# Kernel tuning notes

Hardware: AMD Instinct MI355X
Metric: run time of the kernel (lower is better)

The kernel has to match this reference:

```python
import jax, jax.numpy as jnp
import numpy as np

HEADS = 8
DK = 64            # key_size == size_per_head
NEIGHBORS = 3
KSIZE = 1 + 2 * NEIGHBORS  # 7 (rate=1)


def setup_inputs() -> dict:
    key = jax.random.key(0)
    k1, k2, k3, k4 = jax.random.split(key, 4)
    B, HW, S, D = 2, 64, 256, 512
    inputs = jax.random.normal(k1, (B, HW, S, D), dtype=jnp.float32)
    pos_bias = jax.random.normal(k2, (HEADS, S, KSIZE), dtype=jnp.float32)
    W_qkv = jax.random.normal(k3, (D, 3 * HEADS * DK), dtype=jnp.float32) * 0.02
    W_out = jax.random.normal(k4, (HEADS * DK, D), dtype=jnp.float32) * 0.02
    return {"inputs": inputs, "pos_bias": pos_bias, "W_qkv": W_qkv, "W_out": W_out}


def reference(inputs, pos_bias, W_qkv, W_out):
    B, HW, S, D = inputs.shape
    # qkv projection (no bias), split into q, k, v
    qkv = inputs @ W_qkv                                   # [B,HW,S,3*H*DK]
    q, k, v = jnp.split(qkv, 3, axis=-1)
    q = (q / jnp.sqrt(jnp.float32(DK))).reshape(B, HW, S, HEADS, DK)
    k = k.reshape(B, HW, S, HEADS, DK)
    v = v.reshape(B, HW, S, HEADS, DK)

    # zero-pad keys/values along seq (faithful to F.pad with value=0)
    pad = NEIGHBORS
    kp = jnp.pad(k, ((0, 0), (0, 0), (pad, pad), (0, 0), (0, 0)))
    vp = jnp.pad(v, ((0, 0), (0, 0), (pad, pad), (0, 0), (0, 0)))

    # sliding-window gather: window w for query i covers padded positions i..i+KSIZE-1
    idx = jnp.arange(S)[:, None] + jnp.arange(KSIZE)[None, :]  # [S,KSIZE]
    kw = kp[:, :, idx]                                         # [B,HW,S,KSIZE,H,DK]
    vw = vp[:, :, idx]                                         # [B,HW,S,KSIZE,H,DK]

    # scores over the window
    attn = jnp.einsum('bnshd,bnswhd->bnswh', q, kw)            # [B,HW,S,KSIZE,H]
    # additive positional bias: [H,S,KSIZE] -> [S,KSIZE,H] broadcast
    attn = attn + jnp.transpose(pos_bias, (1, 2, 0))[None, None]
    attn = jax.nn.softmax(attn, axis=-2)                       # softmax over window dim

    out = jnp.einsum('bnswh,bnswhd->bnshd', attn, vw)          # [B,HW,S,H,DK]
    out = out.reshape(B, HW, S, HEADS * DK)
    return out @ W_out
```

## Files before the change

### kernel.cpp

```cpp
#include <hip/hip_runtime.h>
#include <hip/hip_bf16.h>
#include <cstdint>


typedef __bf16 bf16x8 __attribute__((ext_vector_type(8)));
typedef float f32x4 __attribute__((ext_vector_type(4)));

__device__ __forceinline__ uint16_t f2bf(float f) {
    uint32_t u = __builtin_bit_cast(uint32_t, f);
    return (uint16_t)((u + 0x7fffu + ((u >> 16) & 1u)) >> 16);
}
__device__ __forceinline__ float bflo(uint32_t u) { return __builtin_bit_cast(float, u << 16); }
__device__ __forceinline__ float bfhi(uint32_t u) { return __builtin_bit_cast(float, u & 0xffff0000u); }

__device__ __forceinline__ void unpack8(uint4 v, float* f) {
    f[0] = bflo(v.x); f[1] = bfhi(v.x);
    f[2] = bflo(v.y); f[3] = bfhi(v.y);
    f[4] = bflo(v.z); f[5] = bfhi(v.z);
    f[6] = bflo(v.w); f[7] = bfhi(v.w);
}
__device__ __forceinline__ uint32_t pack2(float a, float b) {
    return (uint32_t)f2bf(a) | ((uint32_t)f2bf(b) << 16);
}

#define GLOAD_LDS16(gp, lp)                                                        \
    __builtin_amdgcn_global_load_lds((const __attribute__((address_space(1))) void*)(gp), \
                                     (__attribute__((address_space(3))) void*)(lp), 16, 0, 0)

__device__ __forceinline__ bf16x8 ds_read16(const uint16_t* p) {
    bf16x8 r;
    asm volatile("ds_read_b128 %0, %1"
                 : "=v"(r)
                 : "v"((const __attribute__((address_space(3))) void*)p));
    return r;
}

__global__ void cvt_f32_bf16(const float* __restrict__ in, uint16_t* __restrict__ out, int n8) {
    int i = blockIdx.x * 256 + threadIdx.x;
    if (i >= n8) return;
    const float4* p = (const float4*)in + (size_t)i * 2;
    float4 a = p[0], b = p[1];
    uint4 o;
    o.x = pack2(a.x, a.y);
    o.y = pack2(a.z, a.w);
    o.z = pack2(b.x, b.y);
    o.w = pack2(b.z, b.w);
    *((uint4*)out + i) = o;
}

__global__ void transpose_cvt(const float* __restrict__ in, uint16_t* __restrict__ out,
                              int R, int C) {
    int idx = blockIdx.x * 256 + threadIdx.x;
    if (idx >= R * C) return;
    int r = idx / C;
    int c = idx - r * C;
    out[(size_t)c * R + r] = f2bf(in[idx]);
}

template <bool F32OUT>
__global__ __launch_bounds__(512, 2)
void gemm256(const uint16_t* __restrict__ A, const uint16_t* __restrict__ BT,
             void* __restrict__ Cout, int M, int N, int K) {
    __shared__ __align__(16) uint16_t lds[65536];

    const int tid  = threadIdx.x;
    const int lane = tid & 63;
    const int wv   = tid >> 6;
    const int r    = lane & 15;
    const int quad = lane >> 4;
    const int wr   = wv >> 2;
    const int wc   = wv & 3;
    const long bm0 = (long)blockIdx.x * 256;
    const long bn0 = (long)blockIdx.y * 256;
    const int NT   = K >> 6;

    const int c0 = tid, c1 = tid + 512;
    const int row0 = c0 >> 3, row1 = c1 >> 3;
    const int sw0 = ((c0 & 7) ^ (row0 & 7)) * 8;
    const int sw1 = ((c1 & 7) ^ (row1 & 7)) * 8;
    const uint16_t* pA0 = A  + (bm0 + row0) * (long)K + sw0;
    const uint16_t* pA1 = A  + (bm0 + row1) * (long)K + sw1;
    const uint16_t* pB0 = BT + (bn0 + row0) * (long)K + sw0;
    const uint16_t* pB1 = BT + (bn0 + row1) * (long)K + sw1;
    const long hstep = 128 * (long)K;

#define STAGE_A(b_, h_, t_) do {                                                        \
        GLOAD_LDS16(pA0 + (h_) * hstep + (t_) * 64,                                     \
                    &lds[(b_) * 16384 + (h_) * 8192 + c0 * 8]);                         \
        GLOAD_LDS16(pA1 + (h_) * hstep + (t_) * 64,                                     \
                    &lds[(b_) * 16384 + (h_) * 8192 + c1 * 8]);                         \
    } while (0)
#define STAGE_B(b_, h_, t_) do {                                                        \
        GLOAD_LDS16(pB0 + (h_) * hstep + (t_) * 64,                                     \
                    &lds[32768 + (b_) * 16384 + (h_) * 8192 + c0 * 8]);                 \
        GLOAD_LDS16(pB1 + (h_) * hstep + (t_) * 64,                                     \
                    &lds[32768 + (b_) * 16384 + (h_) * 8192 + c1 * 8]);                 \
    } while (0)

    const int swk0 = ((0 + quad) ^ (r & 7)) * 8;
    const int swk1 = ((4 + quad) ^ (r & 7)) * 8;
    const int arow = (wr * 128 + r) * 64;
    const int brow = (wc * 64 + r) * 64;

#define DS_A(mf_, kk_) ds_read16(&lds[aoff + arow + (mf_) * 1024 + ((kk_) ? swk1 : swk0)])
#define DS_B(nf_, kk_) ds_read16(&lds[boff + brow + (nf_) * 1024 + ((kk_) ? swk1 : swk0)])

#define WAITK4 do { asm volatile("s_waitcnt lgkmcnt(4)" ::: "memory");                  \
                    __builtin_amdgcn_sched_barrier(0); } while (0)
#define WAITK0 do { asm volatile("s_waitcnt lgkmcnt(0)" ::: "memory");                  \
                    __builtin_amdgcn_sched_barrier(0); } while (0)

#define MFMA_CL(mbase_, ar_)                                                            \
    __builtin_amdgcn_s_setprio(1);                                                      \
    _Pragma("unroll")                                                                   \
    for (int kk = 0; kk < 2; ++kk)                                                      \
        _Pragma("unroll")                                                               \
        for (int mi = 0; mi < 2; ++mi)                                                  \
            _Pragma("unroll")                                                           \
            for (int nf = 0; nf < 4; ++nf)                                              \
                acc[(mbase_) + mi][nf] = __builtin_amdgcn_mfma_f32_16x16x32_bf16(       \
                    ar_[mi][kk], bfr[nf][kk], acc[(mbase_) + mi][nf], 0, 0, 0);         \
    __builtin_amdgcn_s_setprio(0);

    f32x4 acc[8][4];
#pragma unroll
    for (int mf = 0; mf < 8; ++mf)
#pragma unroll
        for (int nf = 0; nf < 4; ++nf) acc[mf][nf] = (f32x4){0.f, 0.f, 0.f, 0.f};

    STAGE_A(0, 0, 0); STAGE_A(0, 1, 0);
    STAGE_B(0, 0, 0); STAGE_B(0, 1, 0);
    asm volatile("s_waitcnt vmcnt(0)" ::: "memory");
    __builtin_amdgcn_s_barrier();

    for (int t = 0; t < NT; ++t) {
        const int b    = t & 1;
        const int aoff = b * 16384;
        const int boff = 32768 + b * 16384;
        const bool pf  = (t + 1 < NT);

        bf16x8 bfr[4][2];
        bf16x8 a0[2][2], a1[2][2];

#pragma unroll
        for (int nf = 0; nf < 4; ++nf) { bfr[nf][0] = DS_B(nf, 0); bfr[nf][1] = DS_B(nf, 1); }
        a0[0][0] = DS_A(0, 0); a0[0][1] = DS_A(0, 1);
        a0[1][0] = DS_A(1, 0); a0[1][1] = DS_A(1, 1);
        if (pf) { STAGE_A(b ^ 1, 0, t + 1); STAGE_B(b ^ 1, 0, t + 1); }

        a1[0][0] = DS_A(2, 0); a1[0][1] = DS_A(2, 1);
        a1[1][0] = DS_A(3, 0); a1[1][1] = DS_A(3, 1);
        if (pf) { STAGE_A(b ^ 1, 1, t + 1); STAGE_B(b ^ 1, 1, t + 1); }

        WAITK4;
        MFMA_CL(0, a0)

        a0[0][0] = DS_A(4, 0); a0[0][1] = DS_A(4, 1);
        a0[1][0] = DS_A(5, 0); a0[1][1] = DS_A(5, 1);
        WAITK4;
        MFMA_CL(2, a1)

        a1[0][0] = DS_A(6, 0); a1[0][1] = DS_A(6, 1);
        a1[1][0] = DS_A(7, 0); a1[1][1] = DS_A(7, 1);
        WAITK4;
        MFMA_CL(4, a0)

        WAITK0;
        MFMA_CL(6, a1)

        if (pf) {
            asm volatile("s_waitcnt vmcnt(0)" ::: "memory");
            __builtin_amdgcn_s_barrier();
        }
    }

#pragma unroll
    for (int mf = 0; mf < 8; ++mf) {
#pragma unroll
        for (int i = 0; i < 4; ++i) {
            long m = bm0 + wr * 128 + mf * 16 + quad * 4 + i;
            if (F32OUT) {
                float* crow = (float*)Cout + m * (long)N + bn0 + wc * 64 + r;
#pragma unroll
                for (int nf = 0; nf < 4; ++nf) crow[nf * 16] = acc[mf][nf][i];
            } else {
                uint16_t* crow = (uint16_t*)Cout + m * (long)N + bn0 + wc * 64 + r;
#pragma unroll
                for (int nf = 0; nf < 4; ++nf) crow[nf * 16] = f2bf(acc[mf][nf][i]);
            }
        }
    }
#undef STAGE_A
#undef STAGE_B
#undef DS_A
#undef DS_B
#undef WAITK4
#undef WAITK0
#undef MFMA_CL
}

__global__ __launch_bounds__(256, 2)
void local_attn(const uint16_t* __restrict__ qkv, const float* __restrict__ pb,
                uint16_t* __restrict__ attn) {
    __shared__ __align__(16) uint4 smem[4192];

    const int h  = blockIdx.x & 7;
    const int bn = blockIdx.x >> 3;
    const int s  = threadIdx.x;
    const int tid = threadIdx.x;
    const size_t base = (size_t)bn * 256 * 1536;

    const uint16_t* qrow = qkv + base + (size_t)s * 1536 + h * 64;
    uint4 qc[8];
#pragma unroll
    for (int c = 0; c < 8; ++c) qc[c] = *(const uint4*)(qrow + c * 8);

    if (tid < 96) {
        int a    = tid / 48;
        int rem  = tid - a * 48;
        int hr6  = rem >> 3;
        int c8   = rem & 7;
        int hrow = (hr6 < 3) ? hr6 : (256 + hr6);
        smem[a * 2096 + hrow * 8 + c8] = (uint4){0u, 0u, 0u, 0u};
    }

#pragma unroll
    for (int it = 0; it < 16; ++it) {
        int i   = tid + it * 256;
        int a   = i >> 11;
        int idx = i & 2047;
        int sp  = idx >> 3;
        int cs  = (i & 7) ^ ((sp + 3) & 7);
        const uint16_t* src = qkv + base + (size_t)sp * 1536 + 512 + a * 512 + h * 64 + cs * 8;
        GLOAD_LDS16(src, (uint16_t*)&smem[a * 2096 + (sp + 3) * 8 + (i & 7)]);
    }

    __syncthreads();

    float sc[7];
#pragma unroll
    for (int w = 0; w < 7; ++w) sc[w] = 0.f;

#pragma unroll
    for (int c = 0; c < 8; ++c) {
        float qf[8];
        unpack8(qc[c], qf);
        uint4 kc[7];
#pragma unroll
        for (int w = 0; w < 7; ++w) {
            int hrow = s + w;
            kc[w] = smem[hrow * 8 + (c ^ (hrow & 7))];
        }
#pragma unroll
        for (int w = 0; w < 7; ++w) {
            float kf[8];
            unpack8(kc[w], kf);
#pragma unroll
            for (int j = 0; j < 8; ++j) sc[w] += qf[j] * kf[j];
        }
    }

    const float* pbr = pb + ((size_t)h * 256 + s) * 7;
    float mx = -1e30f;
#pragma unroll
    for (int w = 0; w < 7; ++w) {
        sc[w] = sc[w] * 0.125f + pbr[w];
        mx = fmaxf(mx, sc[w]);
    }
    float p[7], sum = 0.f;
#pragma unroll
    for (int w = 0; w < 7; ++w) {
        p[w] = __expf(sc[w] - mx);
        sum += p[w];
    }
    const float inv = 1.f / sum;
#pragma unroll
    for (int w = 0; w < 7; ++w) p[w] *= inv;

    uint4 ov[8];
#pragma unroll
    for (int c = 0; c < 8; ++c) {
        uint4 vc[7];
#pragma unroll
        for (int w = 0; w < 7; ++w) {
            int hrow = s + w;
            vc[w] = smem[2096 + hrow * 8 + (c ^ (hrow & 7))];
        }
        float o[8] = {0.f, 0.f, 0.f, 0.f, 0.f, 0.f, 0.f, 0.f};
#pragma unroll
        for (int w = 0; w < 7; ++w) {
            float vf[8];
            unpack8(vc[w], vf);
#pragma unroll
            for (int j = 0; j < 8; ++j) o[j] += p[w] * vf[j];
        }
        ov[c].x = pack2(o[0], o[1]);
        ov[c].y = pack2(o[2], o[3]);
        ov[c].z = pack2(o[4], o[5]);
        ov[c].w = pack2(o[6], o[7]);
    }

    uint16_t* orow = attn + ((size_t)(bn * 256 + s)) * 512 + h * 64;
#pragma unroll
    for (int c = 0; c < 8; ++c) *(uint4*)(orow + c * 8) = ov[c];
}

extern "C" void kernel_launch(void* const* d_in, const int* in_sizes, int n_in,
                              void* d_out, int out_size, void* d_ws, size_t ws_size,
                              hipStream_t stream) {
    const float* X    = (const float*)d_in[0];
    const float* pb   = (const float*)d_in[1];
    const float* Wqkv = (const float*)d_in[2];
    const float* Wout = (const float*)d_in[3];
    float* out = (float*)d_out;

    char* ws = (char*)d_ws;
    uint16_t* WqkvT = (uint16_t*)(ws);
    uint16_t* WoutT = (uint16_t*)(ws + 1572864);
    uint16_t* qkvb  = (uint16_t*)(ws + 2097152);
    uint16_t* Xb    = (uint16_t*)(ws + 102760448);
    uint16_t* attnb = Xb;

    cvt_f32_bf16<<<(32768 * 512 / 8 + 255) / 256, 256, 0, stream>>>(X, Xb, 32768 * 512 / 8);
    transpose_cvt<<<(512 * 1536 + 255) / 256, 256, 0, stream>>>(Wqkv, WqkvT, 512, 1536);
    transpose_cvt<<<(512 * 512 + 255) / 256, 256, 0, stream>>>(Wout, WoutT, 512, 512);

    gemm256<false><<<dim3(128, 6), 512, 0, stream>>>(Xb, WqkvT, qkvb, 32768, 1536, 512);
    local_attn<<<1024, 256, 0, stream>>>(qkvb, pb, attnb);
    gemm256<true><<<dim3(128, 2), 512, 0, stream>>>(attnb, WoutT, out, 32768, 512, 512);
}
```

Baseline: 257.0 us.

## Shrink GEMM tiles to 256x128 with K=32 steps and split attention waits

The GEMM changes from 256x256 tiles with K-step 64 to 256x128 tiles with K-step 32. This cuts LDS use from 128KB to 48KB and raises the occupancy target to 4 blocks per CU. It also uses a new swizzle so each LDS row packs two tile rows, and it doubles the grid. In the local attention kernel, Q is loaded with explicit global loads and the barriers are split with vmcnt waits, so V staging can overlap the score computation. The smaller tiles give less reuse per block and more barriers per K.

Result: slower. 264.4 us (+2.9%).

```diff
diff --git a/kernel.cpp b/kernel.cpp
--- a/kernel.cpp
+++ b/kernel.cpp
@@ -32,6 +32,14 @@
     asm volatile("ds_read_b128 %0, %1"
                  : "=v"(r)
                  : "v"((const __attribute__((address_space(3))) void*)p));
+    return r;
+}
+
+__device__ __forceinline__ uint4 gload16(const uint16_t* p) {
+    uint4 r;
+    asm volatile("global_load_dwordx4 %0, %1, off"
+                 : "=v"(r)
+                 : "v"((const __attribute__((address_space(1))) void*)p));
     return r;
 }
 
@@ -58,115 +66,95 @@
 }
 
 template <bool F32OUT>
-__global__ __launch_bounds__(512, 2)
-void gemm256(const uint16_t* __restrict__ A, const uint16_t* __restrict__ BT,
+__global__ __launch_bounds__(512, 4)
+void gemm_mn(const uint16_t* __restrict__ A, const uint16_t* __restrict__ BT,
              void* __restrict__ Cout, int M, int N, int K) {
-    __shared__ __align__(16) uint16_t lds[65536];
+    __shared__ __align__(16) uint16_t lds[24576];
 
     const int tid  = threadIdx.x;
     const int lane = tid & 63;
     const int wv   = tid >> 6;
     const int r    = lane & 15;
     const int quad = lane >> 4;
-    const int wr   = wv >> 2;
-    const int wc   = wv & 3;
+    const int wr   = wv >> 1;
+    const int wc   = wv & 1;
     const long bm0 = (long)blockIdx.x * 256;
-    const long bn0 = (long)blockIdx.y * 256;
-    const int NT   = K >> 6;
-
-    const int c0 = tid, c1 = tid + 512;
-    const int row0 = c0 >> 3, row1 = c1 >> 3;
-    const int sw0 = ((c0 & 7) ^ (row0 & 7)) * 8;
-    const int sw1 = ((c1 & 7) ^ (row1 & 7)) * 8;
-    const uint16_t* pA0 = A  + (bm0 + row0) * (long)K + sw0;
-    const uint16_t* pA1 = A  + (bm0 + row1) * (long)K + sw1;
-    const uint16_t* pB0 = BT + (bn0 + row0) * (long)K + sw0;
-    const uint16_t* pB1 = BT + (bn0 + row1) * (long)K + sw1;
-    const long hstep = 128 * (long)K;
-
-#define STAGE_A(b_, h_, t_) do {                                                        \
-        GLOAD_LDS16(pA0 + (h_) * hstep + (t_) * 64,                                     \
-                    &lds[(b_) * 16384 + (h_) * 8192 + c0 * 8]);                         \
-        GLOAD_LDS16(pA1 + (h_) * hstep + (t_) * 64,                                     \
-                    &lds[(b_) * 16384 + (h_) * 8192 + c1 * 8]);                         \
+    const long bn0 = (long)blockIdx.y * 128;
+    const int NT   = K >> 5;
+
+#define SRC_ROWCOL(d_, row_, col_) do {                                                 \
+        int ln_ = (d_) >> 3, pre_ = ((d_) & 7) ^ (ln_ & 7);                             \
+        row_ = 2 * ln_ + (pre_ >> 2);                                                   \
+        col_ = (pre_ & 3) * 8;                                                          \
     } while (0)
-#define STAGE_B(b_, h_, t_) do {                                                        \
-        GLOAD_LDS16(pB0 + (h_) * hstep + (t_) * 64,                                     \
-                    &lds[32768 + (b_) * 16384 + (h_) * 8192 + c0 * 8]);                 \
-        GLOAD_LDS16(pB1 + (h_) * hstep + (t_) * 64,                                     \
-                    &lds[32768 + (b_) * 16384 + (h_) * 8192 + c1 * 8]);                 \
+    int rA0, cA0, rA1, cA1, rB0, cB0;
+    SRC_ROWCOL(tid,       rA0, cA0);
+    SRC_ROWCOL(tid + 512, rA1, cA1);
+    SRC_ROWCOL(tid,       rB0, cB0);
+    const uint16_t* pA0 = A  + (bm0 + rA0) * (long)K + cA0;
+    const uint16_t* pA1 = A  + (bm0 + rA1) * (long)K + cA1;
+    const uint16_t* pB0 = BT + (bn0 + rB0) * (long)K + cB0;
+#undef SRC_ROWCOL
+
+#define STAGE(b_, t_) do {                                                              \
+        GLOAD_LDS16(pA0 + (t_) * 32, &lds[(b_) * 8192 + tid * 8]);                      \
+        GLOAD_LDS16(pA1 + (t_) * 32, &lds[(b_) * 8192 + (tid + 512) * 8]);              \
+        GLOAD_LDS16(pB0 + (t_) * 32, &lds[16384 + (b_) * 4096 + tid * 8]);              \
     } while (0)
 
-    const int swk0 = ((0 + quad) ^ (r & 7)) * 8;
-    const int swk1 = ((4 + quad) ^ (r & 7)) * 8;
-    const int arow = (wr * 128 + r) * 64;
-    const int brow = (wc * 64 + r) * 64;
-
-#define DS_A(mf_, kk_) ds_read16(&lds[aoff + arow + (mf_) * 1024 + ((kk_) ? swk1 : swk0)])
-#define DS_B(nf_, kk_) ds_read16(&lds[boff + brow + (nf_) * 1024 + ((kk_) ? swk1 : swk0)])
-
-#define WAITK4 do { asm volatile("s_waitcnt lgkmcnt(4)" ::: "memory");                  \
+    const int p_ln  = (((r & 1) << 2) | quad) ^ ((r >> 1) & 7);
+    const int aLane = wr * 2048 + (r >> 1) * 64 + p_ln * 8;
+    const int bLane = 16384 + wc * 2048 + (r >> 1) * 64 + p_ln * 8;
+
+#define DS_A(mf_) ds_read16(&lds[aoff + aLane + (mf_) * 512])
+#define DS_B(nf_) ds_read16(&lds[boff + bLane + (nf_) * 512])
+
+#define WAITK2 do { asm volatile("s_waitcnt lgkmcnt(2)" ::: "memory");                  \
                     __builtin_amdgcn_sched_barrier(0); } while (0)
 #define WAITK0 do { asm volatile("s_waitcnt lgkmcnt(0)" ::: "memory");                  \
                     __builtin_amdgcn_sched_barrier(0); } while (0)
 
-#define MFMA_CL(mbase_, ar_)                                                            \
+#define MFMA_CL(m0_, f0_, f1_)                                                          \
     __builtin_amdgcn_s_setprio(1);                                                      \
     _Pragma("unroll")                                                                   \
-    for (int kk = 0; kk < 2; ++kk)                                                      \
-        _Pragma("unroll")                                                               \
-        for (int mi = 0; mi < 2; ++mi)                                                  \
-            _Pragma("unroll")                                                           \
-            for (int nf = 0; nf < 4; ++nf)                                              \
-                acc[(mbase_) + mi][nf] = __builtin_amdgcn_mfma_f32_16x16x32_bf16(       \
-                    ar_[mi][kk], bfr[nf][kk], acc[(mbase_) + mi][nf], 0, 0, 0);         \
+    for (int nf = 0; nf < 4; ++nf)                                                      \
+        acc[(m0_)][nf] = __builtin_amdgcn_mfma_f32_16x16x32_bf16(f0_, bfr[nf],          \
+                                                                 acc[(m0_)][nf], 0, 0, 0); \
+    _Pragma("unroll")                                                                   \
+    for (int nf = 0; nf < 4; ++nf)                                                      \
+        acc[(m0_) + 1][nf] = __builtin_amdgcn_mfma_f32_16x16x32_bf16(f1_, bfr[nf],      \
+                                                                 acc[(m0_) + 1][nf], 0, 0, 0); \
     __builtin_amdgcn_s_setprio(0);
 
-    f32x4 acc[8][4];
-#pragma unroll
-    for (int mf = 0; mf < 8; ++mf)
+    f32x4 acc[4][4];
+#pragma unroll
+    for (int mf = 0; mf < 4; ++mf)
 #pragma unroll
         for (int nf = 0; nf < 4; ++nf) acc[mf][nf] = (f32x4){0.f, 0.f, 0.f, 0.f};
 
-    STAGE_A(0, 0, 0); STAGE_A(0, 1, 0);
-    STAGE_B(0, 0, 0); STAGE_B(0, 1, 0);
+    STAGE(0, 0);
     asm volatile("s_waitcnt vmcnt(0)" ::: "memory");
     __builtin_amdgcn_s_barrier();
 
     for (int t = 0; t < NT; ++t) {
         const int b    = t & 1;
-        const int aoff = b * 16384;
-        const int boff = 32768 + b * 16384;
+        const int aoff = b * 8192;
+        const int boff = b * 4096;
         const bool pf  = (t + 1 < NT);
 
-        bf16x8 bfr[4][2];
-        bf16x8 a0[2][2], a1[2][2];
-
-#pragma unroll
-        for (int nf = 0; nf < 4; ++nf) { bfr[nf][0] = DS_B(nf, 0); bfr[nf][1] = DS_B(nf, 1); }
-        a0[0][0] = DS_A(0, 0); a0[0][1] = DS_A(0, 1);
-        a0[1][0] = DS_A(1, 0); a0[1][1] = DS_A(1, 1);
-        if (pf) { STAGE_A(b ^ 1, 0, t + 1); STAGE_B(b ^ 1, 0, t + 1); }
-
-        a1[0][0] = DS_A(2, 0); a1[0][1] = DS_A(2, 1);
-        a1[1][0] = DS_A(3, 0); a1[1][1] = DS_A(3, 1);
-        if (pf) { STAGE_A(b ^ 1, 1, t + 1); STAGE_B(b ^ 1, 1, t + 1); }
-
-        WAITK4;
-        MFMA_CL(0, a0)
-
-        a0[0][0] = DS_A(4, 0); a0[0][1] = DS_A(4, 1);
-        a0[1][0] = DS_A(5, 0); a0[1][1] = DS_A(5, 1);
-        WAITK4;
-        MFMA_CL(2, a1)
-
-        a1[0][0] = DS_A(6, 0); a1[0][1] = DS_A(6, 1);
-        a1[1][0] = DS_A(7, 0); a1[1][1] = DS_A(7, 1);
-        WAITK4;
-        MFMA_CL(4, a0)
+        if (pf) STAGE(b ^ 1, t + 1);
+
+        bf16x8 bfr[4], a0, a1, a2, a3;
+#pragma unroll
+        for (int nf = 0; nf < 4; ++nf) bfr[nf] = DS_B(nf);
+        a0 = DS_A(0); a1 = DS_A(1);
+        a2 = DS_A(2); a3 = DS_A(3);
+
+        WAITK2;
+        MFMA_CL(0, a0, a1)
 
         WAITK0;
-        MFMA_CL(6, a1)
+        MFMA_CL(2, a2, a3)
 
         if (pf) {
             asm volatile("s_waitcnt vmcnt(0)" ::: "memory");
@@ -175,10 +163,10 @@
     }
 
 #pragma unroll
-    for (int mf = 0; mf < 8; ++mf) {
+    for (int mf = 0; mf < 4; ++mf) {
 #pragma unroll
         for (int i = 0; i < 4; ++i) {
-            long m = bm0 + wr * 128 + mf * 16 + quad * 4 + i;
+            long m = bm0 + wr * 64 + mf * 16 + quad * 4 + i;
             if (F32OUT) {
                 float* crow = (float*)Cout + m * (long)N + bn0 + wc * 64 + r;
 #pragma unroll
@@ -190,11 +178,10 @@
             }
         }
     }
-#undef STAGE_A
-#undef STAGE_B
+#undef STAGE
 #undef DS_A
 #undef DS_B
-#undef WAITK4
+#undef WAITK2
 #undef WAITK0
 #undef MFMA_CL
 }
@@ -213,7 +200,7 @@
     const uint16_t* qrow = qkv + base + (size_t)s * 1536 + h * 64;
     uint4 qc[8];
 #pragma unroll
-    for (int c = 0; c < 8; ++c) qc[c] = *(const uint4*)(qrow + c * 8);
+    for (int c = 0; c < 8; ++c) qc[c] = gload16(qrow + c * 8);
 
     if (tid < 96) {
         int a    = tid / 48;
@@ -235,7 +222,9 @@
         GLOAD_LDS16(src, (uint16_t*)&smem[a * 2096 + (sp + 3) * 8 + (i & 7)]);
     }
 
-    __syncthreads();
+    asm volatile("s_waitcnt vmcnt(8) lgkmcnt(0)" ::: "memory");
+    __builtin_amdgcn_s_barrier();
+    __builtin_amdgcn_sched_barrier(0);
 
     float sc[7];
 #pragma unroll
@@ -276,6 +265,10 @@
     const float inv = 1.f / sum;
 #pragma unroll
     for (int w = 0; w < 7; ++w) p[w] *= inv;
+
+    asm volatile("s_waitcnt vmcnt(0)" ::: "memory");
+    __builtin_amdgcn_s_barrier();
+    __builtin_amdgcn_sched_barrier(0);
 
     uint4 ov[8];
 #pragma unroll
@@ -325,7 +318,7 @@
     transpose_cvt<<<(512 * 1536 + 255) / 256, 256, 0, stream>>>(Wqkv, WqkvT, 512, 1536);
     transpose_cvt<<<(512 * 512 + 255) / 256, 256, 0, stream>>>(Wout, WoutT, 512, 512);
 
-    gemm256<false><<<dim3(128, 6), 512, 0, stream>>>(Xb, WqkvT, qkvb, 32768, 1536, 512);
+    gemm_mn<false><<<dim3(128, 12), 512, 0, stream>>>(Xb, WqkvT, qkvb, 32768, 1536, 512);
     local_attn<<<1024, 256, 0, stream>>>(qkvb, pb, attnb);
-    gemm256<true><<<dim3(128, 2), 512, 0, stream>>>(attnb, WoutT, out, 32768, 512, 512);
-}
+    gemm_mn<true><<<dim3(128, 4), 512, 0, stream>>>(attnb, WoutT, out, 32768, 512, 512);
+}
```
